# Kernel tuning notes

Hardware: AMD Instinct MI355X
Metric: run time of the kernel (lower is better)

The kernel has to match this reference:

```python
import jax, jax.numpy as jnp
import numpy as np

ALPHA = 1.0
INF = 1e4  # larger than any possible distance in a 256x256 image


def _row_dist_to_zero(x):
    """1D distance along last axis to nearest zero pixel. x: [..., W] (0/1)."""
    W = x.shape[-1]
    idx = jnp.arange(W, dtype=jnp.float32)
    is0 = x == 0
    # nearest zero at-or-before each position
    last0 = jax.lax.cummax(jnp.where(is0, idx, -1.0), axis=x.ndim - 1)
    fwd = jnp.where(last0 >= 0, idx - last0, INF)
    # nearest zero at-or-after each position (suffix max of -idx)
    neg_next0 = jax.lax.cummax(jnp.where(is0, -idx, -INF), axis=x.ndim - 1, reverse=True)
    bwd = jnp.where(neg_next0 > -INF, (-neg_next0) - idx, INF)
    return jnp.minimum(fwd, bwd)


def _edt_2d(target):
    """Exact Euclidean distance transform per [B,C] map: distance from nonzero
    pixels to nearest zero pixel (matches scipy.ndimage.distance_transform_edt)."""
    B, C, H, W = target.shape
    g = _row_dist_to_zero(target)            # [B,C,H,W] distance along width
    g2 = g * g
    i = jnp.arange(H, dtype=jnp.float32)
    dk2 = (i[:, None] - i[None, :]) ** 2     # [H(out), H(k)]
    # dt2[b,c,i,w] = min_k g2[b,c,k,w] + (i-k)^2
    d2 = jnp.min(g2[:, :, None, :, :] + dk2[None, None, :, :, None], axis=3)
    return jnp.sqrt(d2)


def _distance_map(target):
    dist = _edt_2d(target)
    dmax = jnp.max(dist, axis=(-2, -1), keepdims=True)
    return dist / (dmax + 1e-7)


def setup_inputs() -> dict:
    key = jax.random.key(0)
    k1, k2 = jax.random.split(key)
    pred = jax.random.normal(k1, (8, 1, 256, 256), dtype=jnp.float32)
    target = jax.random.randint(k2, (8, 1, 256, 256), 0, 2).astype(jnp.float32)
    return {"pred": pred, "target": target}


def reference(pred, target):
    dist_map = _distance_map(target)
    weight_map = 1.0 + ALPHA * dist_map
    # numerically stable BCE with logits, reduction='none'
    bce = jnp.maximum(pred, 0.0) - pred * target + jnp.log1p(jnp.exp(-jnp.abs(pred)))
    return jnp.mean(weight_map * bce)
```

## Files before the change

### kernel.cpp

```cpp
#include <hip/hip_runtime.h>
#include <math.h>

#define BATCH 8
#define H 256
#define W 256
#define NPIX (BATCH * H * W)
#define NBLK2 1024

__device__ __forceinline__ float bce_logits(float p, float t) {
    return fmaxf(p, 0.0f) - p * t + log1pf(expf(-fabsf(p)));
}

__global__ void __launch_bounds__(256) row_edt(const float* __restrict__ target,
                                               float* __restrict__ g2) {
    __shared__ unsigned long long mlds[4][4];
    const int tid = threadIdx.x;
    const int v = tid >> 6, l = tid & 63;
    const float* imgr = target + (size_t)blockIdx.x * 4 * W;

    #pragma unroll
    for (int j = 0; j < 4; ++j) {
        float t = imgr[j * W + tid];
        unsigned long long m = __ballot(t == 0.0f);
        if (l == 0) mlds[j][v] = m;
    }
    __syncthreads();

    const int p = tid;
    #pragma unroll
    for (int j = 0; j < 4; ++j) {
        unsigned long long mw[4] = {mlds[j][0], mlds[j][1], mlds[j][2], mlds[j][3]};
        int best = 1 << 20;
        #pragma unroll
        for (int w = 0; w < 4; ++w) {
            const int rel = p - (w << 6);
            const unsigned long long m = mw[w];
            unsigned long long mlo = (rel < 0)  ? 0ull
                                   : (rel >= 63) ? m : (m & ((2ull << rel) - 1ull));
            unsigned long long mhi = (rel <= 0) ? m
                                   : (rel > 63)  ? 0ull : (m & (~0ull << rel));
            if (mlo) best = min(best, rel - (63 - __builtin_clzll(mlo)));
            if (mhi) best = min(best, __builtin_ctzll(mhi) - rel);
        }
        float d = (best > 255) ? 1e4f : (float)best;
        g2[(size_t)blockIdx.x * 4 * W + j * W + tid] = d * d;
    }
}

__global__ void __launch_bounds__(256) envelope_bce(
        const float* __restrict__ g2, const float* __restrict__ pred,
        const float* __restrict__ target,
        float* __restrict__ pmx, float* __restrict__ psb, float* __restrict__ psdb) {
    __shared__ float red[3][4];
    const int tid = threadIdx.x;
    const int wv = tid >> 6, l = tid & 63;
    const int b  = blockIdx.x >> 7;
    const int cs = (blockIdx.x >> 5) & 3;
    const int rs = blockIdx.x & 31;
    const int c  = (cs << 6) + l;
    const int i0 = (rs << 3) + (wv << 1);

    const size_t po = ((size_t)(b * H + i0)) * W + c;
    float p0 = pred[po], p1 = pred[po + W];
    float t0 = target[po], t1 = target[po + W];

    const float* gcol = g2 + (size_t)b * H * W + c;

    float acc0 = 3.0e38f, acc1 = 3.0e38f;
    const int P = 10;
    #pragma unroll
    for (int s = 0; s < P; ++s) {
        const int kd = i0 + 1 - s;
        const int ku = i0 + 2 + s;
        float gd = gcol[(size_t)max(kd, 0) * W];
        float gu = gcol[(size_t)min(ku, 255) * W];
        if (kd < 0)   gd = 3.0e38f;
        if (ku > 255) gu = 3.0e38f;
        const float ed0 = (float)(s - 1), ed1 = (float)s;
        const float eu0 = (float)(s + 2), eu1 = (float)(s + 1);
        acc0 = fminf(acc0, fminf(fmaf(ed0, ed0, gd), fmaf(eu0, eu0, gu)));
        acc1 = fminf(acc1, fminf(fmaf(ed1, ed1, gd), fmaf(eu1, eu1, gu)));
    }

    int kd = i0 + 1 - P, ku = i0 + 2 + P;
    float fd0 = (float)(i0 - kd);
    float fu0 = (float)(ku - i0);
    for (;;) {
        float maxacc = fmaxf(acc0, acc1);
        float dn = (float)(i0 - kd);
        float up = (float)(ku - (i0 + 1));
        bool alive = (kd >= 0 && dn * dn <= maxacc) || (ku <= 255 && up * up <= maxacc);
        if (!__any(alive)) break;
        if (kd >= 0) {
            float g = gcol[(size_t)kd * W];
            acc0 = fminf(acc0, fmaf(fd0, fd0, g));
            float fd1 = fd0 + 1.0f;
            acc1 = fminf(acc1, fmaf(fd1, fd1, g));
        }
        if (ku <= 255) {
            float g = gcol[(size_t)ku * W];
            float fu1 = fu0 - 1.0f;
            acc0 = fminf(acc0, fmaf(fu0, fu0, g));
            acc1 = fminf(acc1, fmaf(fu1, fu1, g));
        }
        --kd; ++ku; fd0 += 1.0f; fu0 += 1.0f;
    }

    float mx = fmaxf(acc0, acc1);
    float b0 = bce_logits(p0, t0), b1 = bce_logits(p1, t1);
    float sb  = b0 + b1;
    float sdb = sqrtf(acc0) * b0 + sqrtf(acc1) * b1;

    #pragma unroll
    for (int o = 32; o > 0; o >>= 1) {
        mx  = fmaxf(mx, __shfl_down(mx, o, 64));
        sb  += __shfl_down(sb, o, 64);
        sdb += __shfl_down(sdb, o, 64);
    }
    if (l == 0) { red[0][wv] = mx; red[1][wv] = sb; red[2][wv] = sdb; }
    __syncthreads();
    if (tid == 0) {
        pmx [blockIdx.x] = fmaxf(fmaxf(red[0][0], red[0][1]), fmaxf(red[0][2], red[0][3]));
        psb [blockIdx.x] = (red[1][0] + red[1][1]) + (red[1][2] + red[1][3]);
        psdb[blockIdx.x] = (red[2][0] + red[2][1]) + (red[2][2] + red[2][3]);
    }
}

__global__ void final_reduce(const float* __restrict__ pmx, const float* __restrict__ psb,
                             const float* __restrict__ psdb, float* __restrict__ out) {
    const int tid = threadIdx.x;
    const int img = tid >> 5, j = tid & 31;
    float mx = 0.0f, sb = 0.0f, sdb = 0.0f;
    #pragma unroll
    for (int q = 0; q < 4; ++q) {
        const int e = (img << 7) + j + (q << 5);
        mx  = fmaxf(mx, pmx[e]);
        sb  += psb[e];
        sdb += psdb[e];
    }
    #pragma unroll
    for (int o = 16; o > 0; o >>= 1) {
        mx  = fmaxf(mx, __shfl_down(mx, o, 32));
        sb  += __shfl_down(sb, o, 32);
        sdb += __shfl_down(sdb, o, 32);
    }
    __shared__ float cimg[8], simg[8];
    if (j == 0) {
        cimg[img] = sdb / (sqrtf(mx) + 1e-7f);
        simg[img] = sb;
    }
    __syncthreads();
    if (tid == 0) {
        float tot = 0.0f;
        #pragma unroll
        for (int i = 0; i < 8; ++i) tot += simg[i] + cimg[i];
        out[0] = tot * (1.0f / (float)NPIX);
    }
}

extern "C" void kernel_launch(void* const* d_in, const int* in_sizes, int n_in,
                              void* d_out, int out_size, void* d_ws, size_t ws_size,
                              hipStream_t stream) {
    const float* pred   = (const float*)d_in[0];
    const float* target = (const float*)d_in[1];

    float* g2   = (float*)d_ws;
    float* pmx  = (float*)((char*)d_ws + (size_t)NPIX * sizeof(float));
    float* psb  = pmx + NBLK2;
    float* psdb = psb + NBLK2;

    row_edt<<<BATCH * 64, 256, 0, stream>>>(target, g2);
    envelope_bce<<<NBLK2, 256, 0, stream>>>(g2, pred, target, pmx, psb, psdb);
    final_reduce<<<1, 256, 0, stream>>>(pmx, psb, psdb, (float*)d_out);
}
```

Measured before the change: 65.34 us.

## Fuse row EDT into envelope kernel with shared-memory halo of recomputed rows

Merges the row distance transform into the column envelope/BCE kernel. Each block recomputes squared row distances for a 48-row halo into LDS using wave ballots and a shift-based nearest-zero search, which removes the global g2 buffer and one kernel launch. Rows outside the halo fall back to a slow per-thread global scan of the target row. The cost is redundant row-EDT work across column-slice blocks and a rare, expensive fallback path.

```diff
diff --git a/kernel.cpp b/kernel.cpp
--- a/kernel.cpp
+++ b/kernel.cpp
@@ -6,35 +6,30 @@
 #define W 256
 #define NPIX (BATCH * H * W)
 #define NBLK2 1024
+#define HALO 48
 
 __device__ __forceinline__ float bce_logits(float p, float t) {
     return fmaxf(p, 0.0f) - p * t + log1pf(expf(-fabsf(p)));
 }
 
-__global__ void __launch_bounds__(256) row_edt(const float* __restrict__ target,
-                                               float* __restrict__ g2) {
-    __shared__ unsigned long long mlds[4][4];
-    const int tid = threadIdx.x;
-    const int v = tid >> 6, l = tid & 63;
-    const float* imgr = target + (size_t)blockIdx.x * 4 * W;
-
-    #pragma unroll
-    for (int j = 0; j < 4; ++j) {
-        float t = imgr[j * W + tid];
-        unsigned long long m = __ballot(t == 0.0f);
-        if (l == 0) mlds[j][v] = m;
-    }
-    __syncthreads();
-
-    const int p = tid;
-    #pragma unroll
-    for (int j = 0; j < 4; ++j) {
-        unsigned long long mw[4] = {mlds[j][0], mlds[j][1], mlds[j][2], mlds[j][3]};
-        int best = 1 << 20;
+__device__ __forceinline__ float g2_from_mask(const unsigned long long ww[4], int p) {
+    const int q = p >> 6, r = p & 63;
+    const unsigned long long Wq = ww[q];
+    const unsigned long long Wm = (q > 0) ? ww[q - 1] : 0ull;
+    const unsigned long long Wp = (q < 3) ? ww[q + 1] : 0ull;
+    const unsigned long long down = (Wq << (63 - r)) | ((r == 63) ? 0ull : (Wm >> (r + 1)));
+    const unsigned long long up   = (Wq >> r) | ((r == 0) ? 0ull : (Wp << (64 - r)));
+    int best;
+    if (down | up) {
+        int dd = down ? __builtin_clzll(down) : (1 << 20);
+        int du = up   ? __builtin_ctzll(up)   : (1 << 20);
+        best = min(dd, du);
+    } else {
+        best = 1 << 20;
         #pragma unroll
         for (int w = 0; w < 4; ++w) {
             const int rel = p - (w << 6);
-            const unsigned long long m = mw[w];
+            const unsigned long long m = ww[w];
             unsigned long long mlo = (rel < 0)  ? 0ull
                                    : (rel >= 63) ? m : (m & ((2ull << rel) - 1ull));
             unsigned long long mhi = (rel <= 0) ? m
@@ -42,15 +37,26 @@
             if (mlo) best = min(best, rel - (63 - __builtin_clzll(mlo)));
             if (mhi) best = min(best, __builtin_ctzll(mhi) - rel);
         }
-        float d = (best > 255) ? 1e4f : (float)best;
-        g2[(size_t)blockIdx.x * 4 * W + j * W + tid] = d * d;
     }
+    float d = (best > 255) ? 1e4f : (float)best;
+    return d * d;
 }
 
-__global__ void __launch_bounds__(256) envelope_bce(
-        const float* __restrict__ g2, const float* __restrict__ pred,
-        const float* __restrict__ target,
+__device__ float g2_global_scan(const float* __restrict__ timg, int k, int c) {
+    int best = 1 << 20;
+    for (int q = 0; q < W; ++q)
+        if (timg[(size_t)k * W + q] == 0.0f) {
+            int dd = q > c ? q - c : c - q;
+            best = min(best, dd);
+        }
+    float d = (best > 255) ? 1e4f : (float)best;
+    return d * d;
+}
+
+__global__ void __launch_bounds__(256) edt_bce_mega(
+        const float* __restrict__ target, const float* __restrict__ pred,
         float* __restrict__ pmx, float* __restrict__ psb, float* __restrict__ psdb) {
+    __shared__ float g2h[HALO][64];
     __shared__ float red[3][4];
     const int tid = threadIdx.x;
     const int wv = tid >> 6, l = tid & 63;
@@ -59,12 +65,27 @@
     const int rs = blockIdx.x & 31;
     const int c  = (cs << 6) + l;
     const int i0 = (rs << 3) + (wv << 1);
+    const int hlo = (rs << 3) - 16;
+
+    const float* timg = target + (size_t)b * H * W;
 
     const size_t po = ((size_t)(b * H + i0)) * W + c;
     float p0 = pred[po], p1 = pred[po + W];
-    float t0 = target[po], t1 = target[po + W];
+    float t0 = timg[(size_t)i0 * W + c], t1 = timg[(size_t)(i0 + 1) * W + c];
 
-    const float* gcol = g2 + (size_t)b * H * W + c;
+    for (int h = 0; h < HALO / 4; ++h) {
+        const int hr = hlo + wv * (HALO / 4) + h;
+        const int rr = min(max(hr, 0), H - 1);
+        const float* trow = timg + (size_t)rr * W;
+        unsigned long long ww[4];
+        ww[0] = __ballot(trow[l      ] == 0.0f);
+        ww[1] = __ballot(trow[l +  64] == 0.0f);
+        ww[2] = __ballot(trow[l + 128] == 0.0f);
+        ww[3] = __ballot(trow[l + 192] == 0.0f);
+        float g = g2_from_mask(ww, c);
+        g2h[wv * (HALO / 4) + h][l] = (hr < 0 || hr > H - 1) ? 3.0e38f : g;
+    }
+    __syncthreads();
 
     float acc0 = 3.0e38f, acc1 = 3.0e38f;
     const int P = 10;
@@ -72,10 +93,8 @@
     for (int s = 0; s < P; ++s) {
         const int kd = i0 + 1 - s;
         const int ku = i0 + 2 + s;
-        float gd = gcol[(size_t)max(kd, 0) * W];
-        float gu = gcol[(size_t)min(ku, 255) * W];
-        if (kd < 0)   gd = 3.0e38f;
-        if (ku > 255) gu = 3.0e38f;
+        float gd = g2h[kd - hlo][l];
+        float gu = g2h[ku - hlo][l];
         const float ed0 = (float)(s - 1), ed1 = (float)s;
         const float eu0 = (float)(s + 2), eu1 = (float)(s + 1);
         acc0 = fminf(acc0, fminf(fmaf(ed0, ed0, gd), fmaf(eu0, eu0, gu)));
@@ -89,16 +108,18 @@
         float maxacc = fmaxf(acc0, acc1);
         float dn = (float)(i0 - kd);
         float up = (float)(ku - (i0 + 1));
-        bool alive = (kd >= 0 && dn * dn <= maxacc) || (ku <= 255 && up * up <= maxacc);
+        bool alive = (kd >= 0 && dn * dn <= maxacc) || (ku <= H - 1 && up * up <= maxacc);
         if (!__any(alive)) break;
         if (kd >= 0) {
-            float g = gcol[(size_t)kd * W];
+            int idx = kd - hlo;
+            float g = (idx >= 0) ? g2h[idx][l] : g2_global_scan(timg, kd, c);
             acc0 = fminf(acc0, fmaf(fd0, fd0, g));
             float fd1 = fd0 + 1.0f;
             acc1 = fminf(acc1, fmaf(fd1, fd1, g));
         }
-        if (ku <= 255) {
-            float g = gcol[(size_t)ku * W];
+        if (ku <= H - 1) {
+            int idx = ku - hlo;
+            float g = (idx < HALO) ? g2h[idx][l] : g2_global_scan(timg, ku, c);
             float fu1 = fu0 - 1.0f;
             acc0 = fminf(acc0, fmaf(fu0, fu0, g));
             acc1 = fminf(acc1, fmaf(fu1, fu1, g));
@@ -164,12 +185,10 @@
     const float* pred   = (const float*)d_in[0];
     const float* target = (const float*)d_in[1];
 
-    float* g2   = (float*)d_ws;
-    float* pmx  = (float*)((char*)d_ws + (size_t)NPIX * sizeof(float));
+    float* pmx  = (float*)d_ws;
     float* psb  = pmx + NBLK2;
     float* psdb = psb + NBLK2;
 
-    row_edt<<<BATCH * 64, 256, 0, stream>>>(target, g2);
-    envelope_bce<<<NBLK2, 256, 0, stream>>>(g2, pred, target, pmx, psb, psdb);
+    edt_bce_mega<<<NBLK2, 256, 0, stream>>>(target, pred, pmx, psb, psdb);
     final_reduce<<<1, 256, 0, stream>>>(pmx, psb, psdb, (float*)d_out);
 }
```

New measurement: 66.91 us. 2.4% more time.
